# Kernel tuning notes

Measured on AMD Instinct MI355X. Metric: run time of the kernel, lower is better.

Reference implementation:

```python
import math
import jax, jax.numpy as jnp
import numpy as np

DIM = 512
HEADS = 8
HEAD_DIM = DIM // HEADS


def get_slopes(n):
    def pow2(n):
        start = 2 ** (-2 ** (-(math.log2(n) - 3)))
        return [start * start ** i for i in range(n)]
    if math.log2(n).is_integer():
        return pow2(n)
    c = 2 ** math.floor(math.log2(n))
    return pow2(c) + get_slopes(2 * c)[0::2][: n - c]


def setup_inputs() -> dict:
    key = jax.random.key(0)
    ks = jax.random.split(key, 12)
    b, n, d = 2, 4096, DIM
    s = 1.0 / math.sqrt(d)
    inp = {
        "x": jax.random.normal(ks[0], (b, n, d), jnp.float32),
        # coords in a ~[0,100) spatial range (tile grid coordinates)
        "coords": jax.random.uniform(ks[1], (b, n, 2), jnp.float32) * 100.0,
        "Wq": jax.random.normal(ks[2], (d, d), jnp.float32) * s,
        "bq": jnp.zeros((d,), jnp.float32),
        "Wk": jax.random.normal(ks[3], (d, d), jnp.float32) * s,
        "bk": jnp.zeros((d,), jnp.float32),
        "Wv": jax.random.normal(ks[4], (d, d), jnp.float32) * s,
        "bv": jnp.zeros((d,), jnp.float32),
        "Wp": jax.random.normal(ks[5], (d, d), jnp.float32) * s,
        "bp": jnp.zeros((d,), jnp.float32),
        "slopes": jnp.asarray(get_slopes(HEADS), jnp.float32),  # [h]
    }
    return inp


def reference(x, coords, Wq, bq, Wk, bk, Wv, bv, Wp, bp, slopes):
    b, n_q, d = x.shape
    h, hd = HEADS, HEAD_DIM
    # self-attention: context = x, context_coords = coords
    q = (x @ Wq + bq).reshape(b, n_q, h, hd).transpose(0, 2, 1, 3)  # b h nq hd
    k = (x @ Wk + bk).reshape(b, n_q, h, hd).transpose(0, 2, 1, 3)
    v = (x @ Wv + bv).reshape(b, n_q, h, hd).transpose(0, 2, 1, 3)
    # Euclidean-distance ALiBi bias: [b, h, nq, nk]
    diff = coords[:, :, None, :] - coords[:, None, :, :]          # b nq nk 2
    dist = jnp.sqrt(jnp.sum(diff * diff, axis=-1))                # b nq nk
    bias = -slopes[None, :, None, None] * dist[:, None, :, :]     # b h nq nk
    scores = jnp.einsum("bhqd,bhkd->bhqk", q, k) / math.sqrt(hd) + bias
    attn = jax.nn.softmax(scores, axis=-1)
    out = jnp.einsum("bhqk,bhkd->bhqd", attn, v)
    out = out.transpose(0, 2, 1, 3).reshape(b, n_q, d)
    return out @ Wp + bp
```

## Files before the change

kernel.cpp:

```cpp
#include <hip/hip_runtime.h>
#include <stdint.h>

typedef __bf16 bf16;
typedef __attribute__((ext_vector_type(8))) __bf16 bf16x8;
typedef __attribute__((ext_vector_type(4))) __bf16 bf16x4;
typedef __attribute__((ext_vector_type(4))) float f32x4;

#define DEVFN static __device__ __forceinline__

DEVFN void gload16(const bf16* g, char* l) {
  __builtin_amdgcn_global_load_lds(
      (const __attribute__((address_space(1))) void*)g,
      (__attribute__((address_space(3))) void*)l, 16, 0, 0);
}
DEVFN void gload4(const float* g, char* l) {
  __builtin_amdgcn_global_load_lds(
      (const __attribute__((address_space(1))) void*)g,
      (__attribute__((address_space(3))) void*)l, 4, 0, 0);
}

DEVFN int swz(int row, int kb) { return row * 128 + (kb ^ ((row & 7) << 4)); }

#define PS 9437184LL

__global__ __launch_bounds__(256) void prep_kernel(
    const float* __restrict__ x, const float* __restrict__ Wq,
    const float* __restrict__ Wk, const float* __restrict__ Wv,
    const float* __restrict__ Wp, bf16* __restrict__ xb,
    bf16* __restrict__ Wt, bf16* __restrict__ Wpt) {
  const int64_t tid = blockIdx.x * 256LL + threadIdx.x;
  const int64_t stride = (int64_t)gridDim.x * 256LL;
  for (int64_t i = tid; i < (8192LL * 512) / 4; i += stride) {
    float4 v = ((const float4*)x)[i];
    bf16x4 o = {(bf16)v.x, (bf16)v.y, (bf16)v.z, (bf16)v.w};
    ((bf16x4*)xb)[i] = o;
  }
  for (int64_t i = tid; i < 1536LL * 512; i += stride) {
    int c = (int)(i >> 9), k = (int)(i & 511);
    int wsel = c >> 9, cc = c & 511;
    const float* W = wsel == 0 ? Wq : (wsel == 1 ? Wk : Wv);
    Wt[i] = (bf16)W[k * 512 + cc];
  }
  for (int64_t i = tid; i < 512LL * 512; i += stride) {
    int c = (int)(i >> 9), k = (int)(i & 511);
    Wpt[i] = (bf16)Wp[k * 512 + c];
  }
}

DEVFN void gemm_main(const bf16* __restrict__ A, const bf16* __restrict__ B,
                     int rowA0, int rowB0, char* sA, char* sB, f32x4 acc[4][4],
                     int wr, int wc, int lane, int w) {
#pragma unroll
  for (int m = 0; m < 4; m++)
#pragma unroll
    for (int n = 0; n < 4; n++) acc[m][n] = (f32x4){0.f, 0.f, 0.f, 0.f};
  const int lr = lane >> 3;
  const int kswz = 8 * ((lane & 7) ^ lr);
  for (int k0 = 0; k0 < 512; k0 += 64) {
#pragma unroll
    for (int j = 0; j < 4; j++) {
      const int c = w * 4 + j;
      gload16(A + (rowA0 + c * 8 + lr) * 512 + k0 + kswz, sA + c * 1024);
      gload16(B + (rowB0 + c * 8 + lr) * 512 + k0 + kswz, sB + c * 1024);
    }
    __syncthreads();
    bf16x8 af[4][2], bfv[4][2];
#pragma unroll
    for (int m = 0; m < 4; m++)
#pragma unroll
      for (int kk = 0; kk < 2; kk++) {
        af[m][kk] = *(const bf16x8*)(sA + swz(wr * 64 + m * 16 + (lane & 15),
                                              kk * 64 + (lane >> 4) * 16));
        bfv[m][kk] = *(const bf16x8*)(sB + swz(wc * 64 + m * 16 + (lane & 15),
                                               kk * 64 + (lane >> 4) * 16));
      }
#pragma unroll
    for (int m = 0; m < 4; m++)
#pragma unroll
      for (int n = 0; n < 4; n++)
#pragma unroll
        for (int kk = 0; kk < 2; kk++)
          acc[m][n] = __builtin_amdgcn_mfma_f32_16x16x32_bf16(
              af[m][kk], bfv[n][kk], acc[m][n], 0, 0, 0);
    __syncthreads();
  }
}

__global__ __launch_bounds__(256) void qkv_gemm(
    const bf16* __restrict__ xb, const bf16* __restrict__ Wt,
    const float* __restrict__ bq, const float* __restrict__ bk,
    const float* __restrict__ bv, bf16* __restrict__ Qb, bf16* __restrict__ Kb,
    bf16* __restrict__ Vt) {
  __shared__ __align__(128) char sA[16384];
  __shared__ __align__(128) char sB[16384];
  const int lane = threadIdx.x & 63, w = threadIdx.x >> 6;
  const int wr = w >> 1, wc = w & 1;
  const int rowA0 = blockIdx.y * 128;
  const int colB0 = blockIdx.x * 128;
  f32x4 acc[4][4];
  gemm_main(xb, Wt, rowA0, colB0, sA, sB, acc, wr, wc, lane, w);
  const int which = colB0 >> 9;
  const int cc0 = colB0 & 511;
  const float* bias = which == 0 ? bq : (which == 1 ? bk : bv);
  const float QSCALE = 0.18033688011112042f;
#pragma unroll
  for (int m = 0; m < 4; m++)
#pragma unroll
    for (int n = 0; n < 4; n++)
#pragma unroll
      for (int r = 0; r < 4; r++) {
        int row = rowA0 + wr * 64 + m * 16 + (lane >> 4) * 4 + r;
        int col = cc0 + wc * 64 + n * 16 + (lane & 15);
        float v = acc[m][n][r] + bias[col];
        if (which == 0) {
          Qb[(int64_t)row * 512 + col] = (bf16)(v * QSCALE);
        } else if (which == 1) {
          Kb[(int64_t)row * 512 + col] = (bf16)v;
        } else {
          int b = row >> 12, nn = row & 4095;
          int hh = col >> 6, e = col & 63;
          Vt[(((int64_t)(b * 8 + hh)) * 64 + e) * 4096 + nn] = (bf16)v;
        }
      }
}

__global__ __launch_bounds__(256) void out_gemm(const bf16* __restrict__ Ob,
                                                const bf16* __restrict__ Wpt,
                                                const float* __restrict__ bp,
                                                float* __restrict__ out) {
  __shared__ __align__(128) char sA[16384];
  __shared__ __align__(128) char sB[16384];
  const int lane = threadIdx.x & 63, w = threadIdx.x >> 6;
  const int wr = w >> 1, wc = w & 1;
  const int rowA0 = blockIdx.y * 128;
  const int colB0 = blockIdx.x * 128;
  f32x4 acc[4][4];
  gemm_main(Ob, Wpt, rowA0, colB0, sA, sB, acc, wr, wc, lane, w);
#pragma unroll
  for (int m = 0; m < 4; m++)
#pragma unroll
    for (int n = 0; n < 4; n++)
#pragma unroll
      for (int r = 0; r < 4; r++) {
        int row = rowA0 + wr * 64 + m * 16 + (lane >> 4) * 4 + r;
        int col = colB0 + wc * 64 + n * 16 + (lane & 15);
        out[(int64_t)row * 512 + col] = acc[m][n][r] + bp[col];
      }
}

__global__ __launch_bounds__(512) void attn_kernel(
    const bf16* __restrict__ Qb, const bf16* __restrict__ Kb,
    const bf16* __restrict__ Vt, const float* __restrict__ coords,
    const float* __restrict__ slopes, char* __restrict__ part) {
  __shared__ __align__(128) char sK[2 * 4096];
  __shared__ __align__(128) char sV[2 * 5120];
  __shared__ __align__(128) char sC[2 * 256];
  __shared__ __align__(128) char sP[8 * 1280];

  const int tid = threadIdx.x;
  const int lane = tid & 63, w = tid >> 6;
  const int c = lane & 15, g = lane >> 4;

  const int id = blockIdx.x;
  const int bh = id & 15;
  const int qt = (id >> 4) & 31;
  const int ks = id >> 9;
  const int b = bh >> 3, h = bh & 7;
  const int qw = qt * 128 + w * 16;
  const int bO = b * 4096;
  const int kvs = ks * 2048;

  const float LOG2E = 1.4426950408889634f;
  const float negsl2 = -slopes[h] * LOG2E;

  bf16x8 aq[2];
  {
    int64_t base = ((int64_t)(bO + qw + c)) * 512 + h * 64 + g * 8;
    aq[0] = *(const bf16x8*)(Qb + base);
    aq[1] = *(const bf16x8*)(Qb + base + 32);
  }
  const float* cbf = coords + (int64_t)bO * 2;
  float qcx, qcy;
  {
    float2 qc = ((const float2*)cbf)[qw + c];
    qcx = qc.x;
    qcy = qc.y;
  }

  bf16x8 ones;
#pragma unroll
  for (int jj = 0; jj < 8; jj++) ones[jj] = (bf16)1.0f;

  float m2 = -1e30f;
  f32x4 o[4], osum;
#pragma unroll
  for (int n = 0; n < 4; n++) o[n] = (f32x4){0.f, 0.f, 0.f, 0.f};
  osum = (f32x4){0.f, 0.f, 0.f, 0.f};

  const bf16* Kp = Kb + (int64_t)bO * 512 + h * 64;
  const bf16* Vp = Vt + (int64_t)(b * 8 + h) * 262144;

  auto vstage = [&](int j, int kv0, int bb) {
    const int G = j * 64 + lane;
    const int row = (G * 52429) >> 18;
    int gr = G - row * 5;
    if (gr > 3) gr = 0;
    gload16(Vp + row * 4096 + kv0 + gr * 8, sV + bb * 5120 + j * 1024);
  };
  auto STAGE = [&](int tile, int bb) {
    const int kv0 = kvs + tile * 32;
    if (w < 4) {
      gload16(Kp + (int64_t)(kv0 + w * 8 + (lane >> 3)) * 512 +
                  ((lane & 7) ^ ((lane >> 3) & 7)) * 8,
              sK + bb * 4096 + w * 1024);
    } else {
      vstage(w - 4, kv0, bb);
    }
    if (w == 0) vstage(4, kv0, bb);
    if (w == 1) gload4(cbf + kv0 * 2 + lane, sC + bb * 256);
  };

  STAGE(0, 0);
  __syncthreads();

  char* pwv = sP + w * 1280;
  for (int tt = 0; tt < 64; ++tt) {
    const int bb = tt & 1;
    if (tt + 1 < 64) STAGE(tt + 1, bb ^ 1);

    const char* kb = sK + bb * 4096;
    const char* vb = sV + bb * 5120;
    const char* cbuf = sC + bb * 256;

    bf16x8 kf[2][2];
#pragma unroll
    for (int t = 0; t < 2; t++)
#pragma unroll
      for (int kk = 0; kk < 2; kk++)
        kf[t][kk] = *(const bf16x8*)(kb + (t * 16 + c) * 128 +
                                     (((kk * 4 + g) ^ (c & 7)) * 16));
    float s[2][4];
    __builtin_amdgcn_s_setprio(1);
#pragma unroll
    for (int t = 0; t < 2; t++) {
      f32x4 sa = (f32x4){0.f, 0.f, 0.f, 0.f};
      sa = __builtin_amdgcn_mfma_f32_16x16x32_bf16(kf[t][0], aq[0], sa, 0, 0, 0);
      sa = __builtin_amdgcn_mfma_f32_16x16x32_bf16(kf[t][1], aq[1], sa, 0, 0, 0);
#pragma unroll
      for (int r = 0; r < 4; r++) s[t][r] = sa[r];
    }
    __builtin_amdgcn_s_setprio(0);

#pragma unroll
    for (int t = 0; t < 2; t++) {
      f32x4 ca = *(const f32x4*)(cbuf + 128 * t + 32 * g);
      f32x4 cb2 = *(const f32x4*)(cbuf + 128 * t + 32 * g + 16);
      float dx, dy;
#define DIST1(T, R, CX, CY)                                              \
  dx = qcx - (CX);                                                       \
  dy = qcy - (CY);                                                       \
  s[T][R] = __builtin_fmaf(__builtin_amdgcn_sqrtf(dx * dx + dy * dy),    \
                           negsl2, s[T][R]);
      DIST1(t, 0, ca[0], ca[1])
      DIST1(t, 1, ca[2], ca[3])
      DIST1(t, 2, cb2[0], cb2[1])
      DIST1(t, 3, cb2[2], cb2[3])
#undef DIST1
    }

    float lm = fmaxf(fmaxf(fmaxf(s[0][0], s[0][1]), fmaxf(s[0][2], s[0][3])),
                     fmaxf(fmaxf(s[1][0], s[1][1]), fmaxf(s[1][2], s[1][3])));
    lm = fmaxf(lm, __shfl_xor(lm, 16));
    lm = fmaxf(lm, __shfl_xor(lm, 32));
    if (__any(lm > m2 + 8.f)) {
      float nm = fmaxf(m2, lm);
      float sc = __builtin_amdgcn_exp2f(m2 - nm);
      m2 = nm;
      float scr[4];
#pragma unroll
      for (int r = 0; r < 4; r++)
        scr[r] = __shfl(sc, (lane & 48) | (4 * g + r));
#pragma unroll
      for (int n = 0; n < 4; n++)
#pragma unroll
        for (int r = 0; r < 4; r++) o[n][r] *= scr[r];
#pragma unroll
      for (int r = 0; r < 4; r++) osum[r] *= scr[r];
    }

#pragma unroll
    for (int t = 0; t < 2; t++) {
      bf16x4 pv = {(bf16)__builtin_amdgcn_exp2f(s[t][0] - m2),
                   (bf16)__builtin_amdgcn_exp2f(s[t][1] - m2),
                   (bf16)__builtin_amdgcn_exp2f(s[t][2] - m2),
                   (bf16)__builtin_amdgcn_exp2f(s[t][3] - m2)};
      const int L = 2 * t + (g >> 1);
      *(bf16x4*)(pwv + c * 80 + L * 16 + (g & 1) * 8) = pv;
    }
    bf16x8 pa = *(const bf16x8*)(pwv + c * 80 + g * 16);

    __builtin_amdgcn_s_setprio(1);
#pragma unroll
    for (int n = 0; n < 4; n++) {
      bf16x8 vf = *(const bf16x8*)(vb + (n * 16 + c) * 80 + g * 16);
      o[n] = __builtin_amdgcn_mfma_f32_16x16x32_bf16(pa, vf, o[n], 0, 0, 0);
    }
    osum = __builtin_amdgcn_mfma_f32_16x16x32_bf16(pa, ones, osum, 0, 0, 0);
    __builtin_amdgcn_s_setprio(0);

    __syncthreads();
  }

  float m2r[4];
#pragma unroll
  for (int r = 0; r < 4; r++)
    m2r[r] = __shfl(m2, (lane & 48) | (4 * g + r));
  char* pb0 = part + ks * PS + ((int64_t)bh * 4096 + qw) * 144;
#pragma unroll
  for (int r = 0; r < 4; r++) {
    char* pb = pb0 + (g * 4 + r) * 144;
    if (c == 0) {
      *(float*)pb = m2r[r];
      *((float*)pb + 1) = osum[r];
    }
#pragma unroll
    for (int n = 0; n < 4; n++)
      *(bf16*)(pb + 16 + (n * 16 + c) * 2) = (bf16)o[n][r];
  }
}

__global__ __launch_bounds__(256) void combine_kernel(
    const char* __restrict__ part, bf16* __restrict__ Ob) {
  const int t = blockIdx.x * 256 + threadIdx.x;
  const int row = t >> 6;
  const int e = t & 63;
  const char* p0 = part + (int64_t)row * 144;
  const char* p1 = p0 + PS;
  const float m0 = *(const float*)p0, s0 = *((const float*)p0 + 1);
  const float m1 = *(const float*)p1, s1 = *((const float*)p1 + 1);
  const float o0 = (float)*(const bf16*)(p0 + 16 + e * 2);
  const float o1 = (float)*(const bf16*)(p1 + 16 + e * 2);
  const float m = fmaxf(m0, m1);
  const float w0 = __builtin_amdgcn_exp2f(m0 - m);
  const float w1 = __builtin_amdgcn_exp2f(m1 - m);
  const float res = (o0 * w0 + o1 * w1) / (s0 * w0 + s1 * w1);
  const int bh = row >> 12, q = row & 4095;
  Ob[((int64_t)((bh >> 3) * 4096 + q)) * 512 + (bh & 7) * 64 + e] = (bf16)res;
}

extern "C" void kernel_launch(void* const* d_in, const int* in_sizes, int n_in,
                              void* d_out, int out_size, void* d_ws,
                              size_t ws_size, hipStream_t stream) {
  const float* x = (const float*)d_in[0];
  const float* coords = (const float*)d_in[1];
  const float* Wq = (const float*)d_in[2];
  const float* bq = (const float*)d_in[3];
  const float* Wk = (const float*)d_in[4];
  const float* bk = (const float*)d_in[5];
  const float* Wv = (const float*)d_in[6];
  const float* bv = (const float*)d_in[7];
  const float* Wp = (const float*)d_in[8];
  const float* bp = (const float*)d_in[9];
  const float* slopes = (const float*)d_in[10];

  char* ws = (char*)d_ws;
  bf16* xb = (bf16*)(ws);
  bf16* Wt = (bf16*)(ws + 8388608);
  bf16* Wpt = (bf16*)(ws + 9961472);
  bf16* Qb = (bf16*)(ws + 10485760);
  bf16* Kb = (bf16*)(ws + 18874368);
  bf16* Vt = (bf16*)(ws + 27262976);
  bf16* Ob = (bf16*)(ws + 35651584);
  char* part = ws + 44040192;

  hipLaunchKernelGGL(prep_kernel, dim3(1024), dim3(256), 0, stream, x, Wq, Wk,
                     Wv, Wp, xb, Wt, Wpt);
  hipLaunchKernelGGL(qkv_gemm, dim3(12, 64), dim3(256), 0, stream, xb, Wt, bq,
                     bk, bv, Qb, Kb, Vt);
  hipLaunchKernelGGL(attn_kernel, dim3(1024), dim3(512), 0, stream, Qb, Kb,
                     Vt, coords, slopes, part);
  hipLaunchKernelGGL(combine_kernel, dim3(16384), dim3(256), 0, stream, part,
                     Ob);
  hipLaunchKernelGGL(out_gemm, dim3(4, 64), dim3(256), 0, stream, Ob, Wpt, bp,
                     (float*)d_out);
}
```

Measured before the change: 232.6 us.

## Triple-buffer attention K/V/coord staging with vmcnt waits and single barrier

```diff
diff --git a/kernel.cpp b/kernel.cpp
--- a/kernel.cpp
+++ b/kernel.cpp
@@ -152,9 +152,9 @@
     const bf16* __restrict__ Qb, const bf16* __restrict__ Kb,
     const bf16* __restrict__ Vt, const float* __restrict__ coords,
     const float* __restrict__ slopes, char* __restrict__ part) {
-  __shared__ __align__(128) char sK[2 * 4096];
-  __shared__ __align__(128) char sV[2 * 5120];
-  __shared__ __align__(128) char sC[2 * 256];
+  __shared__ __align__(128) char sK[3 * 4096];
+  __shared__ __align__(128) char sV[3 * 5120];
+  __shared__ __align__(128) char sC[3 * 256];
   __shared__ __align__(128) char sP[8 * 1280];
 
   const int tid = threadIdx.x;
@@ -200,44 +200,61 @@
   const bf16* Kp = Kb + (int64_t)bO * 512 + h * 64;
   const bf16* Vp = Vt + (int64_t)(b * 8 + h) * 262144;
 
-  auto vstage = [&](int j, int kv0, int bb) {
+  auto vaddr = [&](int j) {
     const int G = j * 64 + lane;
     const int row = (G * 52429) >> 18;
     int gr = G - row * 5;
     if (gr > 3) gr = 0;
-    gload16(Vp + row * 4096 + kv0 + gr * 8, sV + bb * 5120 + j * 1024);
+    return Vp + row * 4096 + kvs + gr * 8;
   };
-  auto STAGE = [&](int tile, int bb) {
-    const int kv0 = kvs + tile * 32;
+  const bf16* kq = Kp + (int64_t)(kvs + w * 8 + (lane >> 3)) * 512 +
+                   ((lane & 7) ^ ((lane >> 3) & 7)) * 8;
+  const bf16* vq = vaddr(w & 3);
+  const bf16* vx = vaddr(4);
+  const float* cq = cbf + kvs * 2 + lane;
+
+  auto STAGE = [&](char* kdst, char* vdst, char* cdst) {
     if (w < 4) {
-      gload16(Kp + (int64_t)(kv0 + w * 8 + (lane >> 3)) * 512 +
-                  ((lane & 7) ^ ((lane >> 3) & 7)) * 8,
-              sK + bb * 4096 + w * 1024);
+      gload16(kq, kdst + w * 1024);
+      kq += 32 * 512;
     } else {
-      vstage(w - 4, kv0, bb);
-    }
-    if (w == 0) vstage(4, kv0, bb);
-    if (w == 1) gload4(cbf + kv0 * 2 + lane, sC + bb * 256);
+      gload16(vq, vdst + (w & 3) * 1024);
+      vq += 32;
+    }
+    if (w == 1) {
+      gload4(cq, cdst);
+      cq += 64;
+    } else {
+      gload16(vx, vdst + 4096);
+      vx += 32;
+    }
   };
 
-  STAGE(0, 0);
-  __syncthreads();
+  char *k0 = sK, *k1 = sK + 4096, *k2 = sK + 8192;
+  char *v0 = sV, *v1 = sV + 5120, *v2 = sV + 10240;
+  char *c0 = sC, *c1 = sC + 256, *c2 = sC + 512;
+
+  STAGE(k0, v0, c0);
+  STAGE(k1, v1, c1);
 
   char* pwv = sP + w * 1280;
   for (int tt = 0; tt < 64; ++tt) {
-    const int bb = tt & 1;
-    if (tt + 1 < 64) STAGE(tt + 1, bb ^ 1);
-
-    const char* kb = sK + bb * 4096;
-    const char* vb = sV + bb * 5120;
-    const char* cbuf = sC + bb * 256;
+    if (tt < 63) {
+      asm volatile("s_waitcnt vmcnt(2)" ::: "memory");
+    } else {
+      asm volatile("s_waitcnt vmcnt(0)" ::: "memory");
+    }
+    __builtin_amdgcn_sched_barrier(0);
+    __builtin_amdgcn_s_barrier();
+    __builtin_amdgcn_sched_barrier(0);
+    if (tt + 2 < 64) STAGE(k2, v2, c2);
 
     bf16x8 kf[2][2];
 #pragma unroll
     for (int t = 0; t < 2; t++)
 #pragma unroll
       for (int kk = 0; kk < 2; kk++)
-        kf[t][kk] = *(const bf16x8*)(kb + (t * 16 + c) * 128 +
+        kf[t][kk] = *(const bf16x8*)(k0 + (t * 16 + c) * 128 +
                                      (((kk * 4 + g) ^ (c & 7)) * 16));
     float s[2][4];
     __builtin_amdgcn_s_setprio(1);
@@ -253,8 +270,8 @@
 
 #pragma unroll
     for (int t = 0; t < 2; t++) {
-      f32x4 ca = *(const f32x4*)(cbuf + 128 * t + 32 * g);
-      f32x4 cb2 = *(const f32x4*)(cbuf + 128 * t + 32 * g + 16);
+      f32x4 ca = *(const f32x4*)(c0 + 128 * t + 32 * g);
+      f32x4 cb2 = *(const f32x4*)(c0 + 128 * t + 32 * g + 16);
       float dx, dy;
 #define DIST1(T, R, CX, CY)                                              \
   dx = qcx - (CX);                                                       \
@@ -302,13 +319,15 @@
     __builtin_amdgcn_s_setprio(1);
 #pragma unroll
     for (int n = 0; n < 4; n++) {
-      bf16x8 vf = *(const bf16x8*)(vb + (n * 16 + c) * 80 + g * 16);
+      bf16x8 vf = *(const bf16x8*)(v0 + (n * 16 + c) * 80 + g * 16);
       o[n] = __builtin_amdgcn_mfma_f32_16x16x32_bf16(pa, vf, o[n], 0, 0, 0);
     }
     osum = __builtin_amdgcn_mfma_f32_16x16x32_bf16(pa, ones, osum, 0, 0, 0);
     __builtin_amdgcn_s_setprio(0);
 
-    __syncthreads();
+    char* tk = k0; k0 = k1; k1 = k2; k2 = tk;
+    char* tv = v0; v0 = v1; v1 = v2; v2 = tv;
+    char* tc = c0; c0 = c1; c1 = c2; c2 = tc;
   }
 
   float m2r[4];
```

New measurement: 271.9 us. 1.17x slower.

## Double KV tile size to 64 keys per iteration with XOR-swizzled V and P layouts

Applied to the files above, without the earlier changes.

```diff
diff --git a/kernel.cpp b/kernel.cpp
--- a/kernel.cpp
+++ b/kernel.cpp
@@ -152,10 +152,10 @@
     const bf16* __restrict__ Qb, const bf16* __restrict__ Kb,
     const bf16* __restrict__ Vt, const float* __restrict__ coords,
     const float* __restrict__ slopes, char* __restrict__ part) {
-  __shared__ __align__(128) char sK[2 * 4096];
-  __shared__ __align__(128) char sV[2 * 5120];
-  __shared__ __align__(128) char sC[2 * 256];
-  __shared__ __align__(128) char sP[8 * 1280];
+  __shared__ __align__(128) char sK[2 * 8192];
+  __shared__ __align__(128) char sV[2 * 8192];
+  __shared__ __align__(128) char sC[2 * 512];
+  __shared__ __align__(128) char sP[8 * 2048];
 
   const int tid = threadIdx.x;
   const int lane = tid & 63, w = tid >> 6;
@@ -200,49 +200,48 @@
   const bf16* Kp = Kb + (int64_t)bO * 512 + h * 64;
   const bf16* Vp = Vt + (int64_t)(b * 8 + h) * 262144;
 
-  auto vstage = [&](int j, int kv0, int bb) {
-    const int G = j * 64 + lane;
-    const int row = (G * 52429) >> 18;
-    int gr = G - row * 5;
-    if (gr > 3) gr = 0;
-    gload16(Vp + row * 4096 + kv0 + gr * 8, sV + bb * 5120 + j * 1024);
+  const int gi = w * 64 + lane;
+  const int kr = gi >> 3, kj = gi & 7;
+  const bf16* kq =
+      Kp + (int64_t)(kvs + kr) * 512 + ((kj ^ (kr & 7)) * 8);
+  const bf16* vq = Vp + kr * 4096 + kvs + ((kj ^ (kr & 7)) * 8);
+  const float* cq = cbf + kvs * 2 + (w & 1) * 64 + lane;
+
+  auto STAGE = [&](int bb) {
+    gload16(kq, sK + bb * 8192 + gi * 16);
+    kq += 64 * 512;
+    gload16(vq, sV + bb * 8192 + gi * 16);
+    vq += 64;
+    if (w == 2 || w == 3) {
+      gload4(cq, sC + bb * 512 + (w & 1) * 256);
+      cq += 128;
+    }
   };
-  auto STAGE = [&](int tile, int bb) {
-    const int kv0 = kvs + tile * 32;
-    if (w < 4) {
-      gload16(Kp + (int64_t)(kv0 + w * 8 + (lane >> 3)) * 512 +
-                  ((lane & 7) ^ ((lane >> 3) & 7)) * 8,
-              sK + bb * 4096 + w * 1024);
-    } else {
-      vstage(w - 4, kv0, bb);
-    }
-    if (w == 0) vstage(4, kv0, bb);
-    if (w == 1) gload4(cbf + kv0 * 2 + lane, sC + bb * 256);
-  };
-
-  STAGE(0, 0);
+
+  STAGE(0);
   __syncthreads();
 
-  char* pwv = sP + w * 1280;
-  for (int tt = 0; tt < 64; ++tt) {
+  char* pwv = sP + w * 2048;
+  const int cm = c & 7;
+  for (int tt = 0; tt < 32; ++tt) {
     const int bb = tt & 1;
-    if (tt + 1 < 64) STAGE(tt + 1, bb ^ 1);
-
-    const char* kb = sK + bb * 4096;
-    const char* vb = sV + bb * 5120;
-    const char* cbuf = sC + bb * 256;
-
-    bf16x8 kf[2][2];
-#pragma unroll
-    for (int t = 0; t < 2; t++)
+    if (tt + 1 < 32) STAGE(bb ^ 1);
+
+    const char* kb = sK + bb * 8192;
+    const char* vb = sV + bb * 8192;
+    const char* cb0 = sC + bb * 512;
+
+    bf16x8 kf[4][2];
+#pragma unroll
+    for (int t = 0; t < 4; t++)
 #pragma unroll
       for (int kk = 0; kk < 2; kk++)
         kf[t][kk] = *(const bf16x8*)(kb + (t * 16 + c) * 128 +
-                                     (((kk * 4 + g) ^ (c & 7)) * 16));
-    float s[2][4];
+                                     (((kk * 4 + g) ^ cm) * 16));
+    float s[4][4];
     __builtin_amdgcn_s_setprio(1);
 #pragma unroll
-    for (int t = 0; t < 2; t++) {
+    for (int t = 0; t < 4; t++) {
       f32x4 sa = (f32x4){0.f, 0.f, 0.f, 0.f};
       sa = __builtin_amdgcn_mfma_f32_16x16x32_bf16(kf[t][0], aq[0], sa, 0, 0, 0);
       sa = __builtin_amdgcn_mfma_f32_16x16x32_bf16(kf[t][1], aq[1], sa, 0, 0, 0);
@@ -252,9 +251,9 @@
     __builtin_amdgcn_s_setprio(0);
 
 #pragma unroll
-    for (int t = 0; t < 2; t++) {
-      f32x4 ca = *(const f32x4*)(cbuf + 128 * t + 32 * g);
-      f32x4 cb2 = *(const f32x4*)(cbuf + 128 * t + 32 * g + 16);
+    for (int t = 0; t < 4; t++) {
+      f32x4 ca = *(const f32x4*)(cb0 + 128 * t + 32 * g);
+      f32x4 cb2 = *(const f32x4*)(cb0 + 128 * t + 32 * g + 16);
       float dx, dy;
 #define DIST1(T, R, CX, CY)                                              \
   dx = qcx - (CX);                                                       \
@@ -270,10 +269,13 @@
 
     float lm = fmaxf(fmaxf(fmaxf(s[0][0], s[0][1]), fmaxf(s[0][2], s[0][3])),
                      fmaxf(fmaxf(s[1][0], s[1][1]), fmaxf(s[1][2], s[1][3])));
-    lm = fmaxf(lm, __shfl_xor(lm, 16));
-    lm = fmaxf(lm, __shfl_xor(lm, 32));
+    lm = fmaxf(lm,
+               fmaxf(fmaxf(fmaxf(s[2][0], s[2][1]), fmaxf(s[2][2], s[2][3])),
+                     fmaxf(fmaxf(s[3][0], s[3][1]), fmaxf(s[3][2], s[3][3]))));
     if (__any(lm > m2 + 8.f)) {
-      float nm = fmaxf(m2, lm);
+      float lmf = fmaxf(lm, __shfl_xor(lm, 16));
+      lmf = fmaxf(lmf, __shfl_xor(lmf, 32));
+      float nm = fmaxf(m2, lmf);
       float sc = __builtin_amdgcn_exp2f(m2 - nm);
       m2 = nm;
       float scr[4];
@@ -289,23 +291,28 @@
     }
 
 #pragma unroll
-    for (int t = 0; t < 2; t++) {
+    for (int t = 0; t < 4; t++) {
       bf16x4 pv = {(bf16)__builtin_amdgcn_exp2f(s[t][0] - m2),
                    (bf16)__builtin_amdgcn_exp2f(s[t][1] - m2),
                    (bf16)__builtin_amdgcn_exp2f(s[t][2] - m2),
                    (bf16)__builtin_amdgcn_exp2f(s[t][3] - m2)};
-      const int L = 2 * t + (g >> 1);
-      *(bf16x4*)(pwv + c * 80 + L * 16 + (g & 1) * 8) = pv;
-    }
-    bf16x8 pa = *(const bf16x8*)(pwv + c * 80 + g * 16);
+      *(bf16x4*)(pwv + c * 128 + (((2 * t + (g >> 1)) ^ cm) * 16) +
+                 (g & 1) * 8) = pv;
+    }
+    bf16x8 pa0 = *(const bf16x8*)(pwv + c * 128 + ((g ^ cm) * 16));
+    bf16x8 pa1 = *(const bf16x8*)(pwv + c * 128 + (((4 + g) ^ cm) * 16));
 
     __builtin_amdgcn_s_setprio(1);
 #pragma unroll
     for (int n = 0; n < 4; n++) {
-      bf16x8 vf = *(const bf16x8*)(vb + (n * 16 + c) * 80 + g * 16);
-      o[n] = __builtin_amdgcn_mfma_f32_16x16x32_bf16(pa, vf, o[n], 0, 0, 0);
-    }
-    osum = __builtin_amdgcn_mfma_f32_16x16x32_bf16(pa, ones, osum, 0, 0, 0);
+      const int e = n * 16 + c;
+      bf16x8 vf0 = *(const bf16x8*)(vb + e * 128 + ((g ^ (e & 7)) * 16));
+      bf16x8 vf1 = *(const bf16x8*)(vb + e * 128 + (((4 + g) ^ (e & 7)) * 16));
+      o[n] = __builtin_amdgcn_mfma_f32_16x16x32_bf16(pa0, vf0, o[n], 0, 0, 0);
+      o[n] = __builtin_amdgcn_mfma_f32_16x16x32_bf16(pa1, vf1, o[n], 0, 0, 0);
+    }
+    osum = __builtin_amdgcn_mfma_f32_16x16x32_bf16(pa0, ones, osum, 0, 0, 0);
+    osum = __builtin_amdgcn_mfma_f32_16x16x32_bf16(pa1, ones, osum, 0, 0, 0);
     __builtin_amdgcn_s_setprio(0);
 
     __syncthreads();
```

New measurement: 215.1 us. 1.08x faster.
